# Performance work log

Measured on AMD Instinct MI355X. Metric: run time of the kernel, lower is better.

The kernel has to match this reference:

```python
import jax, jax.numpy as jnp
import numpy as np
from jax import lax

EPS = 1e-5

def _bn_train(x, gamma, beta):
    # BatchNorm2d in training mode: batch stats over (N,H,W), biased variance
    mean = jnp.mean(x, axis=(0, 2, 3), keepdims=True)
    var = jnp.mean((x - mean) ** 2, axis=(0, 2, 3), keepdims=True)
    xhat = (x - mean) * lax.rsqrt(var + EPS)
    return gamma[None, :, None, None] * xhat + beta[None, :, None, None]

def _binact(x):
    # forward: sign(x); backward (STE): identity where |x|<=1, zero elsewhere
    y = jnp.where(jnp.abs(x) > 1.0, lax.stop_gradient(x), x)
    return y + lax.stop_gradient(jnp.sign(y) - y)

def _binconv(x, w, padding):
    # per-output-channel alpha = mean(|w|) over (in,kh,kw); w_bin = sign(w)*alpha with STE
    alpha = jnp.mean(jnp.abs(w), axis=(1, 2, 3), keepdims=True)
    w_bin = lax.stop_gradient(jnp.sign(w) * alpha - w) + w
    return lax.conv_general_dilated(
        x, w_bin, window_strides=(1, 1),
        padding=[(padding, padding), (padding, padding)],
        dimension_numbers=("NCHW", "OIHW", "NCHW"))

def setup_inputs() -> dict:
    key = jax.random.key(0)
    ks = jax.random.split(key, 10)
    B, Cin, Cout, H, W, T = 32, 128, 256, 64, 64, 512
    x = jax.random.normal(ks[0], (B, Cin, H, W), jnp.float32)
    t = jax.random.normal(ks[1], (B, T), jnp.float32)
    # conv weights, kaiming-ish scale
    w1 = jax.random.normal(ks[2], (Cout, Cin, 3, 3), jnp.float32) * (1.0 / np.sqrt(Cin * 9))
    w2 = jax.random.normal(ks[3], (Cout, Cout, 3, 3), jnp.float32) * (1.0 / np.sqrt(Cout * 9))
    wskip = jax.random.normal(ks[4], (Cout, Cin, 1, 1), jnp.float32) * (1.0 / np.sqrt(Cin))
    gamma1 = 1.0 + 0.1 * jax.random.normal(ks[5], (Cin,), jnp.float32)
    beta1 = 0.1 * jax.random.normal(ks[6], (Cin,), jnp.float32)
    gamma2 = 1.0 + 0.1 * jax.random.normal(ks[7], (Cout,), jnp.float32)
    beta2 = 0.1 * jax.random.normal(ks[8], (Cout,), jnp.float32)
    tw = jax.random.normal(ks[9], (Cout, T), jnp.float32) * (1.0 / np.sqrt(T))
    tb = jnp.zeros((Cout,), jnp.float32)
    return {"x": x, "t": t, "w1": w1, "w2": w2, "wskip": wskip,
            "gamma1": gamma1, "beta1": beta1, "gamma2": gamma2, "beta2": beta2,
            "tw": tw, "tb": tb}

def reference(x, t, w1, w2, wskip, gamma1, beta1, gamma2, beta2, tw, tb):
    h = _binconv(_binact(_bn_train(x, gamma1, beta1)), w1, padding=1)
    temb = t @ tw.T + tb                      # [B, Cout]
    h = h + temb[:, :, None, None]
    h = _binconv(_binact(_bn_train(h, gamma2, beta2)), w2, padding=1)
    return h + _binconv(x, wskip, padding=0)
```

## Files before the change

kernel.cpp:

```cpp
#include <hip/hip_runtime.h>
#include <stdint.h>

typedef unsigned short u16;
typedef uint8_t u8;
typedef __attribute__((ext_vector_type(8))) short short8;
typedef __attribute__((ext_vector_type(4))) float f32x4;
typedef __attribute__((ext_vector_type(4))) int i32x4;

#define EPSF 1e-5f
#define LGKM0 asm volatile("s_waitcnt lgkmcnt(0)" ::: "memory")
#define VM0   asm volatile("s_waitcnt vmcnt(0)" ::: "memory")
#define VM4   asm volatile("s_waitcnt vmcnt(4)" ::: "memory")
#define BAR   __builtin_amdgcn_s_barrier()
#define GLL(src, dst) __builtin_amdgcn_global_load_lds(                     \
    (const __attribute__((address_space(1))) void*)(src),                   \
    (__attribute__((address_space(3))) void*)(dst), 16, 0, 0)

__device__ __forceinline__ u16 f2bf(float f) {
  uint32_t u = __float_as_uint(f);
  u += 0x7FFFu + ((u >> 16) & 1u);
  return (u16)(u >> 16);
}
__device__ __forceinline__ u8 sgn8(float y) {
  return y > 0.f ? (u8)1 : (y < 0.f ? (u8)0xFF : (u8)0);
}

__global__ void bn1_stage1(const float* __restrict__ x, float* __restrict__ p1) {
  int c = blockIdx.x >> 2, s = blockIdx.x & 3;
  int tid = threadIdx.x;
  float sum = 0.f, sq = 0.f;
  for (int n = s * 8; n < s * 8 + 8; ++n) {
    const f32x4* bp = (const f32x4*)(x + (((size_t)(n * 128 + c)) << 12));
    #pragma unroll 4
    for (int i = tid; i < 1024; i += 256) {
      f32x4 v = bp[i];
      sum += v[0] + v[1] + v[2] + v[3];
      sq  += v[0]*v[0] + v[1]*v[1] + v[2]*v[2] + v[3]*v[3];
    }
  }
  __shared__ float rs[256], rq[256];
  rs[tid] = sum; rq[tid] = sq; __syncthreads();
  for (int st = 128; st > 0; st >>= 1) {
    if (tid < st) { rs[tid] += rs[tid + st]; rq[tid] += rq[tid + st]; }
    __syncthreads();
  }
  if (tid == 0) { p1[blockIdx.x] = rs[0]; p1[512 + blockIdx.x] = rq[0]; }
}

__global__ void bn1_stage2(const float* __restrict__ p1, const float* __restrict__ g,
                           const float* __restrict__ b, float* __restrict__ sc,
                           float* __restrict__ off) {
  int c = threadIdx.x;
  float s = 0.f, q = 0.f;
  for (int k = 0; k < 4; ++k) { s += p1[c * 4 + k]; q += p1[512 + c * 4 + k]; }
  float mean = s * (1.f / 131072.f);
  float var  = q * (1.f / 131072.f) - mean * mean;
  float is = rsqrtf(var + EPSF);
  float scv = g[c] * is;
  sc[c] = scv;
  off[c] = b[c] - mean * scv;
}

__global__ void bn2_stage2b(const float* __restrict__ pS, const float* __restrict__ pQ,
                            const float* __restrict__ g, const float* __restrict__ bb,
                            float* __restrict__ sc, float* __restrict__ off) {
  int o = blockIdx.x, t = threadIdx.x;
  __shared__ float rs[256], rq[256];
  float s = 0.f, q = 0.f;
  #pragma unroll
  for (int k = 0; k < 8; ++k) {
    size_t j = t + k * 256;
    s += pS[j * 256 + o];
    q += pQ[j * 256 + o];
  }
  rs[t] = s; rq[t] = q; __syncthreads();
  for (int st = 128; st > 0; st >>= 1) {
    if (t < st) { rs[t] += rs[t + st]; rq[t] += rq[t + st]; }
    __syncthreads();
  }
  if (t == 0) {
    float mean = rs[0] * (1.f / 131072.f);
    float var  = rq[0] * (1.f / 131072.f) - mean * mean;
    float is = rsqrtf(var + EPSF);
    float scv = g[o] * is;
    sc[o] = scv;
    off[o] = bb[o] - mean * scv;
  }
}

__device__ __forceinline__ float blk_reduce(float v, float* red) {
  int t = threadIdx.x;
  red[t] = v; __syncthreads();
  for (int st = 128; st > 0; st >>= 1) {
    if (t < st) red[t] += red[t + st];
    __syncthreads();
  }
  float r = red[0]; __syncthreads();
  return r;
}

__global__ void prep_weights(const float* __restrict__ w1, const float* __restrict__ w2,
                             const float* __restrict__ wsk, u8* __restrict__ w1s,
                             u8* __restrict__ w2s, u16* __restrict__ wskB,
                             float* __restrict__ alpha1, float* __restrict__ alpha2) {
  int o = blockIdx.x, t = threadIdx.x;
  int rg = o >> 6, ol = o & 63;
  __shared__ float red[256];
  float s = 0.f;
  for (int j = t; j < 1152; j += 256) s += fabsf(w1[(size_t)o * 1152 + j]);
  float a1 = blk_reduce(s, red) * (1.f / 1152.f);
  if (t == 0) alpha1[o] = a1;
  for (int j = t; j < 1152; j += 256) {
    int st = j >> 6, k = j & 63;
    int tap = st >> 1, cc = st & 1;
    int ch = cc * 64 + k;
    int g = (ol << 2) + ((k >> 4) ^ (ol & 3));
    w1s[(size_t)st * 16384 + rg * 4096 + g * 16 + (k & 15)] =
        sgn8(w1[(size_t)o * 1152 + ch * 9 + tap]);
  }
  s = 0.f;
  for (int j = t; j < 2304; j += 256) s += fabsf(w2[(size_t)o * 2304 + j]);
  float a2 = blk_reduce(s, red) * (1.f / 2304.f);
  if (t == 0) alpha2[o] = a2;
  for (int j = t; j < 2304; j += 256) {
    int st = j >> 6, k = j & 63;
    int c2 = st / 18, r = st % 18, tap = r >> 1, cc = r & 1;
    int ch = c2 * 128 + cc * 64 + k;
    int g = (ol << 2) + ((k >> 4) ^ (ol & 3));
    w2s[(size_t)st * 16384 + rg * 4096 + g * 16 + (k & 15)] =
        sgn8(w2[(size_t)o * 2304 + ch * 9 + tap]);
  }
  s = 0.f;
  for (int j = t; j < 128; j += 256) s += fabsf(wsk[o * 128 + j]);
  float ask = blk_reduce(s, red) * (1.f / 128.f);
  float ratio = ask / a2;
  for (int j = t; j < 128; j += 256) {
    int e = j >> 6, k = j & 63;
    float w = wsk[o * 128 + j];
    float v = w > 0.f ? ratio : (w < 0.f ? -ratio : 0.f);
    wskB[(size_t)e * 16384 + o * 64 + k] = f2bf(v);
  }
}

__global__ void temb_k(const float* __restrict__ t, const float* __restrict__ tw,
                       const float* __restrict__ tb, float* __restrict__ temb) {
  int bb = blockIdx.x, o = threadIdx.x;
  __shared__ float tl[512];
  tl[o] = t[bb * 512 + o];
  tl[o + 256] = t[bb * 512 + 256 + o];
  __syncthreads();
  float acc = tb[o];
  #pragma unroll 8
  for (int k = 0; k < 512; ++k) acc += tl[k] * tw[(size_t)o * 512 + k];
  temb[bb * 256 + o] = acc;
}

__global__ void border_zero(u8* __restrict__ Abuf) {
  u8* plane = Abuf + (size_t)blockIdx.x * 557568;
  int tid = threadIdx.x;
  i32x4 z = {};
  for (int idx = tid; idx < 260; idx += 256) {
    int row, px;
    if (idx < 66) { row = 0; px = idx; }
    else if (idx < 132) { row = 65; px = idx - 66; }
    else { int e = idx - 132; row = 1 + (e >> 1); px = (e & 1) * 65; }
    u8* p = plane + (size_t)(row * 66 + px) * 128;
    #pragma unroll
    for (int i = 0; i < 8; ++i) *(i32x4*)(p + i * 16) = z;
  }
}

__global__ void binact1(const float* __restrict__ x, const float* __restrict__ sc,
                        const float* __restrict__ off, u8* __restrict__ a1p,
                        u16* __restrict__ xb) {
  int b = blockIdx.x >> 6, y = blockIdx.x & 63, tid = threadIdx.x;
  __shared__ u8  ls[64 * 144];
  __shared__ u16 lx[64 * 136];
  int c = tid >> 1, x0 = (tid & 1) * 32;
  const float* src = x + (((size_t)(b * 128 + c)) << 12) + y * 64 + x0;
  float s0 = sc[c], o0 = off[c];
  #pragma unroll
  for (int i = 0; i < 32; i += 4) {
    f32x4 v = *(const f32x4*)(src + i);
    #pragma unroll
    for (int j = 0; j < 4; ++j) {
      int xc = x0 + i + j;
      float yv = s0 * v[j] + o0;
      ls[xc * 144 + c] = sgn8(yv);
      lx[xc * 136 + c] = f2bf(v[j]);
    }
  }
  __syncthreads();
  int xx = tid >> 2, cg = (tid & 3) * 32;
  u8*  pdst = a1p + ((size_t)b * 4356 + (y + 1) * 66 + xx + 1) * 128 + cg;
  u16* xdst = xb + ((size_t)blockIdx.x * 64 + xx) * 128 + cg;
  *(i32x4*)(pdst)      = *(const i32x4*)&ls[xx * 144 + cg];
  *(i32x4*)(pdst + 16) = *(const i32x4*)&ls[xx * 144 + cg + 16];
  #pragma unroll
  for (int i = 0; i < 32; i += 8)
    *(i32x4*)(xdst + i) = *(const i32x4*)&lx[xx * 136 + cg + i];
}

__global__ void binact2(const float* __restrict__ h, const float* __restrict__ sc,
                        const float* __restrict__ off, u8* __restrict__ a2p) {
  int b = blockIdx.x >> 6, y = blockIdx.x & 63, tid = threadIdx.x;
  __shared__ float s_sc[256], s_off[256];
  s_sc[tid] = sc[tid]; s_off[tid] = off[tid];
  __syncthreads();
  const f32x4* src = (const f32x4*)(h + (size_t)blockIdx.x * 16384);
  #pragma unroll 4
  for (int i = tid; i < 4096; i += 256) {
    f32x4 v = src[i];
    int px = i >> 6, c0 = (i & 63) * 4;
    int c2 = c0 >> 7, chm = c0 & 127;
    uint32_t p = (uint32_t)sgn8(s_sc[c0 + 0] * v[0] + s_off[c0 + 0]) |
                 ((uint32_t)sgn8(s_sc[c0 + 1] * v[1] + s_off[c0 + 1]) << 8) |
                 ((uint32_t)sgn8(s_sc[c0 + 2] * v[2] + s_off[c0 + 2]) << 16) |
                 ((uint32_t)sgn8(s_sc[c0 + 3] * v[3] + s_off[c0 + 3]) << 24);
    u8* dst = a2p + ((size_t)(b * 2 + c2) * 4356 + (y + 1) * 66 + px + 1) * 128 + chm;
    *(uint32_t*)dst = p;
  }
}

template <int NCHUNK, bool SKIP, bool ADD_TEMB, bool STATS, bool DIRECT>
__global__ __launch_bounds__(256, 2) void convk(
    const u8* __restrict__ Apl, const u16* __restrict__ xb,
    const u8* __restrict__ wS, const u16* __restrict__ wskB,
    const float* __restrict__ alpha, const float* __restrict__ temb,
    float* __restrict__ outp, float* __restrict__ pS, float* __restrict__ pQ) {
  constexpr int NS = NCHUNK * 18;
  __shared__ u8 smem[66560];
  u8* lA = smem;
  u8* lB = smem + 25344;
  const int tid = threadIdx.x;
  const int lane = tid & 63, wn = tid >> 6;
  const int kq = lane >> 4, li = lane & 15;

  const int bid = blockIdx.x;
  const int tile = (bid & 7) * 256 + (bid >> 3);
  const int m0 = tile * 64;
  const int b = tile >> 6, y = tile & 63;

  auto issueB = [&](int s) {
    const u8* src = wS + (size_t)s * 16384 + wn * 4096 + lane * 16;
    u8* dst = lB + (s & 1) * 16384 + wn * 4096;
    #pragma unroll
    for (int i = 0; i < 4; ++i) GLL(src + i * 1024, dst + i * 1024);
  };

  auto winLoad = [&](int c) {
    const u8* gp = Apl + (size_t)(b * NCHUNK + c) * 557568 + (size_t)y * 8448;
    #pragma unroll
    for (int k = 0; k < 6; ++k) {
      int g = tid + k * 256;
      int row = g / 528, rem = g - row * 528;
      int px = rem >> 3, sl = rem & 7;
      const u8* src = gp + (size_t)(row * 66 + px) * 128 + ((sl ^ (px & 7)) << 4);
      u8* dst = lA + (size_t)((tid & ~63) + k * 256) * 16;
      GLL(src, dst);
    }
    if (tid < 48) {
      int g = 1536 + tid;
      int rem = g - 1056;
      int px = rem >> 3, sl = rem & 7;
      const u8* src = gp + (size_t)(2 * 66 + px) * 128 + ((sl ^ (px & 7)) << 4);
      GLL(src, lA + (size_t)1536 * 16);
    }
  };

  const u8* pA[3][2];
  #pragma unroll
  for (int dx = 0; dx < 3; ++dx)
    #pragma unroll
    for (int cc = 0; cc < 2; ++cc)
      pA[dx][cc] = lA + (li + dx) * 128 +
                   ((((cc << 2) + kq) ^ ((li + dx) & 7)) << 4);
  const u8* pB = lB + wn * 4096 + li * 64 + ((kq ^ (li & 3)) << 4);

  i32x4 acc[4][4] = {};

  auto compute = [&](int dy, int dx, int cc, int buf) {
    i32x4 av[4], bv[4];
    #pragma unroll
    for (int f = 0; f < 4; ++f)
      av[f] = *(const i32x4*)(pA[dx][cc] + dy * 8448 + f * 2048);
    #pragma unroll
    for (int f = 0; f < 4; ++f)
      bv[f] = *(const i32x4*)(pB + buf * 16384 + f * 1024);
    __builtin_amdgcn_s_setprio(1);
    #pragma unroll
    for (int mf = 0; mf < 4; ++mf)
      #pragma unroll
      for (int nf = 0; nf < 4; ++nf)
        acc[mf][nf] = __builtin_amdgcn_mfma_i32_16x16x64_i8(
            av[mf], bv[nf], acc[mf][nf], 0, 0, 0);
    __builtin_amdgcn_s_setprio(0);
  };

  winLoad(0);
  issueB(0);
  issueB(1);
  VM4;
  BAR;

  #pragma unroll
  for (int s = 0; s < NS; ++s) {
    if (NCHUNK > 1 && s > 0 && (s % 18) == 0) {
      LGKM0; BAR;
      winLoad(s / 18);
      VM0; BAR;
    }
    const int t = s % 18, cc = t & 1, tap = t >> 1;
    if (s + 2 < NS) { VM4; } else { VM0; }
    compute(tap / 3, tap % 3, cc, s & 1);
    LGKM0;
    if (s + 2 < NS) issueB(s + 2);
  }

  f32x4 facc[4][4];
  if constexpr (SKIP) {
    #pragma unroll
    for (int mf = 0; mf < 4; ++mf)
      #pragma unroll
      for (int nf = 0; nf < 4; ++nf)
        #pragma unroll
        for (int r = 0; r < 4; ++r)
          facc[mf][nf][r] = (float)acc[mf][nf][r];
    const u8* pAs[2];
    const u8* pBs[2];
    #pragma unroll
    for (int ks = 0; ks < 2; ++ks) {
      pAs[ks] = lA + li * 128 + ((((ks << 2) + kq) ^ (li & 7)) << 4);
      pBs[ks] = lB + (wn * 64 + li) * 128 + ((((ks << 2) + kq) ^ (li & 7)) << 4);
    }
    LGKM0; BAR;
    #pragma unroll
    for (int e = 0; e < 2; ++e) {
      #pragma unroll
      for (int k = 0; k < 2; ++k) {
        int g = tid + k * 256;
        int m = g >> 3, sl = g & 7;
        const u8* src = (const u8*)xb + (size_t)(m0 + m) * 256 + e * 128 +
                        ((sl ^ (m & 7)) << 4);
        u8* dst = lA + (size_t)((tid & ~63) + k * 256) * 16;
        GLL(src, dst);
      }
      i32x4 rS[8];
      const i32x4* gs = (const i32x4*)((const u8*)wskB + (size_t)e * 32768) + tid;
      #pragma unroll
      for (int k = 0; k < 8; ++k) rS[k] = gs[k * 256];
      VM0;
      #pragma unroll
      for (int k = 0; k < 8; ++k) {
        int g = tid + k * 256;
        int o = g >> 3, sl = g & 7;
        *(i32x4*)(lB + o * 128 + ((sl ^ (o & 7)) << 4)) = rS[k];
      }
      LGKM0; BAR;
      #pragma unroll
      for (int ks = 0; ks < 2; ++ks) {
        short8 av[4], bv[4];
        #pragma unroll
        for (int f = 0; f < 4; ++f) av[f] = *(const short8*)(pAs[ks] + f * 2048);
        #pragma unroll
        for (int f = 0; f < 4; ++f) bv[f] = *(const short8*)(pBs[ks] + f * 2048);
        __builtin_amdgcn_s_setprio(1);
        #pragma unroll
        for (int mf = 0; mf < 4; ++mf)
          #pragma unroll
          for (int nf = 0; nf < 4; ++nf)
            facc[mf][nf] = __builtin_amdgcn_mfma_f32_16x16x32_bf16(
                av[mf], bv[ks * 4 + nf - ks * 4 + nf == nf ? nf : nf], facc[mf][nf], 0, 0, 0);
        __builtin_amdgcn_s_setprio(0);
      }
      if (e == 0) { LGKM0; BAR; }
    }
  }

  const int cb = wn * 64 + li;

  if constexpr (STATS) {
    float als[4], tas[4];
    #pragma unroll
    for (int nf = 0; nf < 4; ++nf) {
      int o = cb + nf * 16;
      als[nf] = alpha[o];
      tas[nf] = ADD_TEMB ? temb[b * 256 + o] : 0.f;
    }
    float ps[4] = {0.f, 0.f, 0.f, 0.f}, pq[4] = {0.f, 0.f, 0.f, 0.f};
    #pragma unroll
    for (int nf = 0; nf < 4; ++nf)
      #pragma unroll
      for (int mf = 0; mf < 4; ++mf)
        #pragma unroll
        for (int r = 0; r < 4; ++r) {
          float v = (float)acc[mf][nf][r] * als[nf] + tas[nf];
          ps[nf] += v; pq[nf] += v * v;
        }
    #pragma unroll
    for (int nf = 0; nf < 4; ++nf) {
      ps[nf] += __shfl_xor(ps[nf], 16); ps[nf] += __shfl_xor(ps[nf], 32);
      pq[nf] += __shfl_xor(pq[nf], 16); pq[nf] += __shfl_xor(pq[nf], 32);
    }
    if (lane < 16) {
      #pragma unroll
      for (int nf = 0; nf < 4; ++nf) {
        pS[(size_t)bid * 256 + wn * 64 + nf * 16 + lane] = ps[nf];
        pQ[(size_t)bid * 256 + wn * 64 + nf * 16 + lane] = pq[nf];
      }
    }
    __syncthreads();
    float* ld = (float*)smem;
    {
      int colg0_base = cb >> 2, c3 = li & 3;
      #pragma unroll
      for (int nf = 0; nf < 4; ++nf) {
        int colg0 = colg0_base + nf * 4;
        #pragma unroll
        for (int mf = 0; mf < 4; ++mf)
          #pragma unroll
          for (int r = 0; r < 4; ++r) {
            int rloc = mf * 16 + 4 * kq + r;
            float v = (float)acc[mf][nf][r] * als[nf] + tas[nf];
            ld[rloc * 256 + ((colg0 ^ kq) << 2) + c3] = v;
          }
      }
    }
    __syncthreads();
    #pragma unroll
    for (int it = 0; it < 16; ++it) {
      int flat = tid + it * 256;
      int row = flat >> 6, c4 = flat & 63;
      int c4p = c4 ^ ((row >> 2) & 3);
      f32x4 v = *(const f32x4*)&ld[row * 256 + c4p * 4];
      *(f32x4*)(outp + (size_t)(m0 + row) * 256 + c4 * 4) = v;
    }
  } else if constexpr (DIRECT) {
    float* tb2 = (float*)lA;
    float* obase = outp + (((size_t)(b * 256)) << 12) + (m0 & 4095);
    __syncthreads();
    #pragma unroll 1
    for (int c4 = 0; c4 < 4; ++c4) {
      if (wn == c4) {
        #pragma unroll
        for (int nf = 0; nf < 4; ++nf) {
          float al = alpha[c4 * 64 + nf * 16 + li];
          #pragma unroll
          for (int mf = 0; mf < 4; ++mf) {
            int cs = (li + nf * 16) ^ ((mf >> 1) & 3);
            #pragma unroll
            for (int r = 0; r < 4; ++r)
              tb2[(mf * 16 + 4 * kq + r) * 65 + cs] = facc[mf][nf][r] * al;
          }
        }
      }
      __syncthreads();
      #pragma unroll
      for (int it = 0; it < 4; ++it) {
        int flat = tid + it * 256;
        int ch = flat >> 4, mg = flat & 15;
        int chs = ch ^ ((mg >> 3) & 3);
        f32x4 v;
        #pragma unroll
        for (int e = 0; e < 4; ++e) v[e] = tb2[(mg * 4 + e) * 65 + chs];
        *(f32x4*)(obase + (((size_t)(c4 * 64 + ch)) << 12) + mg * 4) = v;
      }
      __syncthreads();
    }
  }
}

extern "C" void kernel_launch(void* const* d_in, const int* in_sizes, int n_in,
                              void* d_out, int out_size, void* d_ws, size_t ws_size,
                              hipStream_t stream) {
  const float* x      = (const float*)d_in[0];
  const float* t      = (const float*)d_in[1];
  const float* w1     = (const float*)d_in[2];
  const float* w2     = (const float*)d_in[3];
  const float* wskip  = (const float*)d_in[4];
  const float* gamma1 = (const float*)d_in[5];
  const float* beta1  = (const float*)d_in[6];
  const float* gamma2 = (const float*)d_in[7];
  const float* beta2  = (const float*)d_in[8];
  const float* tw     = (const float*)d_in[9];
  const float* tb     = (const float*)d_in[10];
  float* out = (float*)d_out;

  uint8_t* base = (uint8_t*)d_ws;
  size_t off = 0;
  auto alloc = [&](size_t bytes) {
    void* p = base + off;
    off += (bytes + 255) & ~(size_t)255;
    return p;
  };
  u8* Abuf     = (u8*)alloc((size_t)96 * 557568);
  u8* a1p      = Abuf;
  u8* a2p      = Abuf + (size_t)32 * 557568;
  u16* xb      = (u16*)alloc((size_t)131072 * 128 * 2);
  float* h     = (float*)alloc((size_t)131072 * 256 * 4);
  u8* w1s      = (u8*)alloc((size_t)18 * 16384);
  u8* w2s      = (u8*)alloc((size_t)36 * 16384);
  u16* wskB    = (u16*)alloc((size_t)2 * 16384 * 2);
  float* temb  = (float*)alloc(32 * 256 * 4);
  float* alpha1 = (float*)alloc(256 * 4);
  float* alpha2 = (float*)alloc(256 * 4);
  float* p1    = (float*)alloc(1024 * 4);
  float* pS    = (float*)alloc((size_t)2048 * 256 * 4);
  float* pQ    = (float*)alloc((size_t)2048 * 256 * 4);
  float* sc1   = (float*)alloc(128 * 4);
  float* off1  = (float*)alloc(128 * 4);
  float* sc2   = (float*)alloc(256 * 4);
  float* off2  = (float*)alloc(256 * 4);

  border_zero<<<96, 256, 0, stream>>>(Abuf);

  bn1_stage1<<<512, 256, 0, stream>>>(x, p1);
  bn1_stage2<<<1, 128, 0, stream>>>(p1, gamma1, beta1, sc1, off1);
  prep_weights<<<256, 256, 0, stream>>>(w1, w2, wskip, w1s, w2s, wskB, alpha1, alpha2);
  temb_k<<<32, 256, 0, stream>>>(t, tw, tb, temb);
  binact1<<<2048, 256, 0, stream>>>(x, sc1, off1, a1p, xb);

  convk<1, false, true, true, false><<<2048, 256, 0, stream>>>(
      a1p, xb, w1s, (const u16*)nullptr, alpha1, temb, h, pS, pQ);

  bn2_stage2b<<<256, 256, 0, stream>>>(pS, pQ, gamma2, beta2, sc2, off2);
  binact2<<<2048, 256, 0, stream>>>(h, sc2, off2, a2p);

  convk<2, true, false, false, true><<<2048, 256, 0, stream>>>(
      a2p, xb, w2s, wskB, alpha2, (const float*)nullptr, out,
      (float*)nullptr, (float*)nullptr);

  (void)in_sizes; (void)n_in; (void)out_size; (void)ws_size;
}
```

Baseline: 289.0 us.

## Split activation planes into 64-channel chunks to cut LDS and raise occupancy

```diff
diff --git a/kernel.cpp b/kernel.cpp
--- a/kernel.cpp
+++ b/kernel.cpp
@@ -112,9 +112,9 @@
   if (t == 0) alpha1[o] = a1;
   for (int j = t; j < 1152; j += 256) {
     int st = j >> 6, k = j & 63;
-    int tap = st >> 1, cc = st & 1;
+    int cc = st / 9, tap = st % 9;
     int ch = cc * 64 + k;
-    int g = (ol << 2) + ((k >> 4) ^ (ol & 3));
+    int g = (ol << 2) + ((k >> 4) ^ ((ol >> 1) & 3));
     w1s[(size_t)st * 16384 + rg * 4096 + g * 16 + (k & 15)] =
         sgn8(w1[(size_t)o * 1152 + ch * 9 + tap]);
   }
@@ -124,9 +124,9 @@
   if (t == 0) alpha2[o] = a2;
   for (int j = t; j < 2304; j += 256) {
     int st = j >> 6, k = j & 63;
-    int c2 = st / 18, r = st % 18, tap = r >> 1, cc = r & 1;
-    int ch = c2 * 128 + cc * 64 + k;
-    int g = (ol << 2) + ((k >> 4) ^ (ol & 3));
+    int c4 = st / 9, tap = st % 9;
+    int ch = c4 * 64 + k;
+    int g = (ol << 2) + ((k >> 4) ^ ((ol >> 1) & 3));
     w2s[(size_t)st * 16384 + rg * 4096 + g * 16 + (k & 15)] =
         sgn8(w2[(size_t)o * 2304 + ch * 9 + tap]);
   }
@@ -156,7 +156,7 @@
 }
 
 __global__ void border_zero(u8* __restrict__ Abuf) {
-  u8* plane = Abuf + (size_t)blockIdx.x * 557568;
+  u8* plane = Abuf + (size_t)blockIdx.x * 278784;
   int tid = threadIdx.x;
   i32x4 z = {};
   for (int idx = tid; idx < 260; idx += 256) {
@@ -164,9 +164,9 @@
     if (idx < 66) { row = 0; px = idx; }
     else if (idx < 132) { row = 65; px = idx - 66; }
     else { int e = idx - 132; row = 1 + (e >> 1); px = (e & 1) * 65; }
-    u8* p = plane + (size_t)(row * 66 + px) * 128;
-    #pragma unroll
-    for (int i = 0; i < 8; ++i) *(i32x4*)(p + i * 16) = z;
+    u8* p = plane + (size_t)(row * 66 + px) * 64;
+    #pragma unroll
+    for (int i = 0; i < 4; ++i) *(i32x4*)(p + i * 16) = z;
   }
 }
 
@@ -192,7 +192,8 @@
   }
   __syncthreads();
   int xx = tid >> 2, cg = (tid & 3) * 32;
-  u8*  pdst = a1p + ((size_t)b * 4356 + (y + 1) * 66 + xx + 1) * 128 + cg;
+  int cc = cg >> 6, ch0 = cg & 63;
+  u8*  pdst = a1p + ((size_t)(b * 2 + cc) * 4356 + (y + 1) * 66 + xx + 1) * 64 + ch0;
   u16* xdst = xb + ((size_t)blockIdx.x * 64 + xx) * 128 + cg;
   *(i32x4*)(pdst)      = *(const i32x4*)&ls[xx * 144 + cg];
   *(i32x4*)(pdst + 16) = *(const i32x4*)&ls[xx * 144 + cg + 16];
@@ -212,26 +213,26 @@
   for (int i = tid; i < 4096; i += 256) {
     f32x4 v = src[i];
     int px = i >> 6, c0 = (i & 63) * 4;
-    int c2 = c0 >> 7, chm = c0 & 127;
+    int c4 = c0 >> 6, chm = c0 & 63;
     uint32_t p = (uint32_t)sgn8(s_sc[c0 + 0] * v[0] + s_off[c0 + 0]) |
                  ((uint32_t)sgn8(s_sc[c0 + 1] * v[1] + s_off[c0 + 1]) << 8) |
                  ((uint32_t)sgn8(s_sc[c0 + 2] * v[2] + s_off[c0 + 2]) << 16) |
                  ((uint32_t)sgn8(s_sc[c0 + 3] * v[3] + s_off[c0 + 3]) << 24);
-    u8* dst = a2p + ((size_t)(b * 2 + c2) * 4356 + (y + 1) * 66 + px + 1) * 128 + chm;
+    u8* dst = a2p + ((size_t)(b * 4 + c4) * 4356 + (y + 1) * 66 + px + 1) * 64 + chm;
     *(uint32_t*)dst = p;
   }
 }
 
 template <int NCHUNK, bool SKIP, bool ADD_TEMB, bool STATS, bool DIRECT>
-__global__ __launch_bounds__(256, 2) void convk(
+__global__ __launch_bounds__(256, 3) void convk(
     const u8* __restrict__ Apl, const u16* __restrict__ xb,
     const u8* __restrict__ wS, const u16* __restrict__ wskB,
     const float* __restrict__ alpha, const float* __restrict__ temb,
     float* __restrict__ outp, float* __restrict__ pS, float* __restrict__ pQ) {
-  constexpr int NS = NCHUNK * 18;
-  __shared__ u8 smem[66560];
+  constexpr int NS = NCHUNK * 9;
+  __shared__ u8 smem[45440];
   u8* lA = smem;
-  u8* lB = smem + 25344;
+  u8* lB = smem + 12672;
   const int tid = threadIdx.x;
   const int lane = tid & 63, wn = tid >> 6;
   const int kq = lane >> 4, li = lane & 15;
@@ -249,41 +250,37 @@
   };
 
   auto winLoad = [&](int c) {
-    const u8* gp = Apl + (size_t)(b * NCHUNK + c) * 557568 + (size_t)y * 8448;
-    #pragma unroll
-    for (int k = 0; k < 6; ++k) {
+    const u8* gp = Apl + (size_t)(b * NCHUNK + c) * 278784 + (size_t)y * 4224;
+    #pragma unroll
+    for (int k = 0; k < 3; ++k) {
       int g = tid + k * 256;
-      int row = g / 528, rem = g - row * 528;
-      int px = rem >> 3, sl = rem & 7;
-      const u8* src = gp + (size_t)(row * 66 + px) * 128 + ((sl ^ (px & 7)) << 4);
+      int row = g / 264, rem = g - row * 264;
+      int px = rem >> 2, sl = rem & 3;
+      const u8* src = gp + (size_t)(row * 66 + px) * 64 + ((sl ^ ((px >> 1) & 3)) << 4);
       u8* dst = lA + (size_t)((tid & ~63) + k * 256) * 16;
       GLL(src, dst);
     }
-    if (tid < 48) {
-      int g = 1536 + tid;
-      int rem = g - 1056;
-      int px = rem >> 3, sl = rem & 7;
-      const u8* src = gp + (size_t)(2 * 66 + px) * 128 + ((sl ^ (px & 7)) << 4);
-      GLL(src, lA + (size_t)1536 * 16);
+    if (tid < 24) {
+      int rem = 240 + tid;
+      int px = rem >> 2, sl = rem & 3;
+      const u8* src = gp + (size_t)(2 * 66 + px) * 64 + ((sl ^ ((px >> 1) & 3)) << 4);
+      GLL(src, lA + (size_t)768 * 16);
     }
   };
 
-  const u8* pA[3][2];
+  const u8* pA[3];
   #pragma unroll
   for (int dx = 0; dx < 3; ++dx)
-    #pragma unroll
-    for (int cc = 0; cc < 2; ++cc)
-      pA[dx][cc] = lA + (li + dx) * 128 +
-                   ((((cc << 2) + kq) ^ ((li + dx) & 7)) << 4);
-  const u8* pB = lB + wn * 4096 + li * 64 + ((kq ^ (li & 3)) << 4);
+    pA[dx] = lA + (li + dx) * 64 + ((kq ^ (((li + dx) >> 1) & 3)) << 4);
+  const u8* pB = lB + wn * 4096 + li * 64 + ((kq ^ ((li >> 1) & 3)) << 4);
 
   i32x4 acc[4][4] = {};
 
-  auto compute = [&](int dy, int dx, int cc, int buf) {
+  auto compute = [&](int dy, int dx, int buf) {
     i32x4 av[4], bv[4];
     #pragma unroll
     for (int f = 0; f < 4; ++f)
-      av[f] = *(const i32x4*)(pA[dx][cc] + dy * 8448 + f * 2048);
+      av[f] = *(const i32x4*)(pA[dx] + dy * 4224 + f * 1024);
     #pragma unroll
     for (int f = 0; f < 4; ++f)
       bv[f] = *(const i32x4*)(pB + buf * 16384 + f * 1024);
@@ -305,14 +302,14 @@
 
   #pragma unroll
   for (int s = 0; s < NS; ++s) {
-    if (NCHUNK > 1 && s > 0 && (s % 18) == 0) {
+    if (NCHUNK > 1 && s > 0 && (s % 9) == 0) {
       LGKM0; BAR;
-      winLoad(s / 18);
+      winLoad(s / 9);
       VM0; BAR;
     }
-    const int t = s % 18, cc = t & 1, tap = t >> 1;
+    const int tap = s % 9;
     if (s + 2 < NS) { VM4; } else { VM0; }
-    compute(tap / 3, tap % 3, cc, s & 1);
+    compute(tap / 3, tap % 3, s & 1);
     LGKM0;
     if (s + 2 < NS) issueB(s + 2);
   }
@@ -370,7 +367,7 @@
           #pragma unroll
           for (int nf = 0; nf < 4; ++nf)
             facc[mf][nf] = __builtin_amdgcn_mfma_f32_16x16x32_bf16(
-                av[mf], bv[ks * 4 + nf - ks * 4 + nf == nf ? nf : nf], facc[mf][nf], 0, 0, 0);
+                av[mf], bv[nf], facc[mf][nf], 0, 0, 0);
         __builtin_amdgcn_s_setprio(0);
       }
       if (e == 0) { LGKM0; BAR; }
@@ -411,32 +408,36 @@
     }
     __syncthreads();
     float* ld = (float*)smem;
-    {
-      int colg0_base = cb >> 2, c3 = li & 3;
-      #pragma unroll
-      for (int nf = 0; nf < 4; ++nf) {
-        int colg0 = colg0_base + nf * 4;
-        #pragma unroll
-        for (int mf = 0; mf < 4; ++mf)
+    const int c3 = li & 3;
+    #pragma unroll 1
+    for (int half = 0; half < 2; ++half) {
+      #pragma unroll
+      for (int mf2 = 0; mf2 < 2; ++mf2) {
+        int mf = half * 2 + mf2;
+        #pragma unroll
+        for (int nf = 0; nf < 4; ++nf) {
+          int colg0 = (cb >> 2) + nf * 4;
           #pragma unroll
           for (int r = 0; r < 4; ++r) {
-            int rloc = mf * 16 + 4 * kq + r;
+            int rloc = mf2 * 16 + 4 * kq + r;
             float v = (float)acc[mf][nf][r] * als[nf] + tas[nf];
             ld[rloc * 256 + ((colg0 ^ kq) << 2) + c3] = v;
           }
-      }
-    }
-    __syncthreads();
-    #pragma unroll
-    for (int it = 0; it < 16; ++it) {
-      int flat = tid + it * 256;
-      int row = flat >> 6, c4 = flat & 63;
-      int c4p = c4 ^ ((row >> 2) & 3);
-      f32x4 v = *(const f32x4*)&ld[row * 256 + c4p * 4];
-      *(f32x4*)(outp + (size_t)(m0 + row) * 256 + c4 * 4) = v;
+        }
+      }
+      __syncthreads();
+      #pragma unroll
+      for (int it = 0; it < 8; ++it) {
+        int flat = tid + it * 256;
+        int row = flat >> 6, c4 = flat & 63;
+        int c4p = c4 ^ ((row >> 2) & 3);
+        f32x4 v = *(const f32x4*)&ld[row * 256 + c4p * 4];
+        *(f32x4*)(outp + (size_t)(m0 + half * 32 + row) * 256 + c4 * 4) = v;
+      }
+      __syncthreads();
     }
   } else if constexpr (DIRECT) {
-    float* tb2 = (float*)lA;
+    float* tb2 = (float*)smem;
     float* obase = outp + (((size_t)(b * 256)) << 12) + (m0 & 4095);
     __syncthreads();
     #pragma unroll 1
@@ -493,9 +494,9 @@
     off += (bytes + 255) & ~(size_t)255;
     return p;
   };
-  u8* Abuf     = (u8*)alloc((size_t)96 * 557568);
+  u8* Abuf     = (u8*)alloc((size_t)192 * 278784);
   u8* a1p      = Abuf;
-  u8* a2p      = Abuf + (size_t)32 * 557568;
+  u8* a2p      = Abuf + (size_t)64 * 278784;
   u16* xb      = (u16*)alloc((size_t)131072 * 128 * 2);
   float* h     = (float*)alloc((size_t)131072 * 256 * 4);
   u8* w1s      = (u8*)alloc((size_t)18 * 16384);
@@ -512,7 +513,7 @@
   float* sc2   = (float*)alloc(256 * 4);
   float* off2  = (float*)alloc(256 * 4);
 
-  border_zero<<<96, 256, 0, stream>>>(Abuf);
+  border_zero<<<192, 256, 0, stream>>>(Abuf);
 
   bn1_stage1<<<512, 256, 0, stream>>>(x, p1);
   bn1_stage2<<<1, 128, 0, stream>>>(p1, gamma1, beta1, sc1, off1);
@@ -520,13 +521,13 @@
   temb_k<<<32, 256, 0, stream>>>(t, tw, tb, temb);
   binact1<<<2048, 256, 0, stream>>>(x, sc1, off1, a1p, xb);
 
-  convk<1, false, true, true, false><<<2048, 256, 0, stream>>>(
+  convk<2, false, true, true, false><<<2048, 256, 0, stream>>>(
       a1p, xb, w1s, (const u16*)nullptr, alpha1, temb, h, pS, pQ);
 
   bn2_stage2b<<<256, 256, 0, stream>>>(pS, pQ, gamma2, beta2, sc2, off2);
   binact2<<<2048, 256, 0, stream>>>(h, sc2, off2, a2p);
 
-  convk<2, true, false, false, true><<<2048, 256, 0, stream>>>(
+  convk<4, true, false, false, true><<<2048, 256, 0, stream>>>(
       a2p, xb, w2s, wskB, alpha2, (const float*)nullptr, out,
       (float*)nullptr, (float*)nullptr);
 
```

New measurement: 601.2 us. 2.08x slower.
